# Optimization experiments

Measured on AMD Instinct MI355X. Metric: run time of the kernel, lower is better.

## Reference

```python
import jax, jax.numpy as jnp
import numpy as np


def setup_inputs() -> dict:
    key = jax.random.key(0)
    k1, k2, k3, k4 = jax.random.split(key, 4)
    B, M, S, Q = 128, 200, 20, 20
    H, V, D = 3, 50000, 128  # max_hops, num_vocab, embedding_dim
    story = jax.random.randint(k1, (B, M, S), 0, V)
    query = jax.random.randint(k2, (B, Q), 0, V)
    # (max_hops+1) embedding tables, init normal(0, 0.1) as in torch code
    E = jax.random.normal(k3, (H + 1, V, D), dtype=jnp.float32) * 0.1
    # (max_hops+1) temporal encodings [max_story_size, D], normal(0, 0.1)
    T = jax.random.normal(k4, (H + 1, M, D), dtype=jnp.float32) * 0.1
    return {"story": story, "query": query, "E": E, "T": T}


def reference(story, query, E, T):
    max_hops = E.shape[0] - 1
    # u1 = sum over query tokens of B-embedding (hop-0 table)
    u = jnp.sum(E[0][query], axis=1)  # [B, D]
    for hop in range(max_hops):
        # memory: A-embed story, sum over words, add temporal encoding
        m = jnp.sum(E[hop][story], axis=2) + T[hop]        # [B, M, D]
        # attention over memories (legacy F.softmax on 2D -> dim=1)
        uTm = jnp.einsum('bmd,bd->bm', m, u)               # [B, M]
        proba = jax.nn.softmax(uTm, axis=1)
        # output memory representation
        c = jnp.sum(E[hop + 1][story], axis=2) + T[hop + 1]  # [B, M, D]
        o = jnp.einsum('bm,bmd->bd', proba, c)             # [B, D]
        u = u + o
    ahat = u @ E[-1].T  # [B, V]
    return ahat, jax.nn.softmax(ahat, axis=1)
```

## Files before the change

kernel.cpp:

```cpp
#include <hip/hip_runtime.h>
#include <float.h>


constexpr int Bn = 128;
constexpr int Mn = 200;
constexpr int Sn = 20;
constexpr int Qn = 20;
constexpr int Hn = 3;
constexpr int Vn = 50000;
constexpr int Dn = 128;
constexpr int CH = 100;

constexpr size_t MSUM_ELEMS = (size_t)(Hn + 1) * Bn * Mn * Dn;

__global__ __launch_bounds__(256)
void msum_kernel(const int* __restrict__ story, const float* __restrict__ E,
                 const float* __restrict__ T, float* __restrict__ msum) {
    int slot = threadIdx.x >> 5;
    int l    = threadIdx.x & 31;
    int row  = blockIdx.x * 8 + slot;
    int t    = row / (Bn * Mn);
    int rem  = row - t * (Bn * Mn);
    int b    = rem / Mn;
    int m    = rem - b * Mn;

    const int* st = story + (b * Mn + m) * Sn;
    const float4* Tv = (const float4*)(T) + (size_t)(t * Mn + m) * 32;
    const float4* Et = (const float4*)(E) + (size_t)t * Vn * 32;

    float4 acc = Tv[l];
    #pragma unroll
    for (int s = 0; s < Sn; ++s) {
        float4 e = Et[(size_t)st[s] * 32 + l];
        acc.x += e.x; acc.y += e.y; acc.z += e.z; acc.w += e.w;
    }
    ((float4*)msum)[(size_t)row * 32 + l] = acc;
}

__global__ __launch_bounds__(1024)
void hops_kernel(const int* __restrict__ query, const float* __restrict__ E,
                 const float* __restrict__ msum, float* __restrict__ ufin) {
    __shared__ float u[Dn];
    __shared__ float sc[Mn];
    __shared__ float op[8 * Dn];
    __shared__ float red[16];
    __shared__ float bc[2];

    const int b    = blockIdx.x;
    const int tid  = threadIdx.x;
    const int wave = tid >> 6;
    const int lane = tid & 63;
    const int d    = tid & (Dn - 1);
    const int g    = tid >> 7;

    if (tid < Dn) {
        float acc = 0.f;
        const int* q = query + b * Qn;
        #pragma unroll
        for (int j = 0; j < Qn; ++j)
            acc += E[(size_t)q[j] * Dn + tid];
        u[tid] = acc;
    }
    __syncthreads();

    for (int hop = 0; hop < Hn; ++hop) {
        const float* mrow = msum + ((size_t)hop * Bn + b) * (size_t)(Mn * Dn);
        float ul = u[lane], uh = u[lane + 64];

        for (int mm = wave; mm < Mn / 2; mm += 16) {
            const float* r0 = mrow + (2 * mm) * Dn;
            const float* r1 = r0 + Dn;
            float p0 = r0[lane] * ul + r0[lane + 64] * uh;
            float p1 = r1[lane] * ul + r1[lane + 64] * uh;
            #pragma unroll
            for (int off = 32; off; off >>= 1) {
                p0 += __shfl_down(p0, off, 64);
                p1 += __shfl_down(p1, off, 64);
            }
            if (lane == 0) { sc[2 * mm] = p0; sc[2 * mm + 1] = p1; }
        }
        __syncthreads();

        float v = (tid < Mn) ? sc[tid] : -FLT_MAX;
        float mx = v;
        #pragma unroll
        for (int off = 32; off; off >>= 1) mx = fmaxf(mx, __shfl_down(mx, off, 64));
        if (lane == 0) red[wave] = mx;
        __syncthreads();
        if (tid == 0) {
            float m0 = red[0];
            #pragma unroll
            for (int i = 1; i < 16; ++i) m0 = fmaxf(m0, red[i]);
            bc[0] = m0;
        }
        __syncthreads();
        float rmax = bc[0];
        float e = (tid < Mn) ? expf(v - rmax) : 0.f;
        float sm = e;
        #pragma unroll
        for (int off = 32; off; off >>= 1) sm += __shfl_down(sm, off, 64);
        if (lane == 0) red[wave] = sm;
        __syncthreads();
        if (tid == 0) {
            float s = 0.f;
            #pragma unroll
            for (int i = 0; i < 16; ++i) s += red[i];
            bc[1] = s;
        }
        __syncthreads();
        float inv = 1.f / bc[1];
        if (tid < Mn) sc[tid] = e * inv;
        __syncthreads();

        const float* crow = msum + ((size_t)(hop + 1) * Bn + b) * (size_t)(Mn * Dn);
        float acc = 0.f;
        for (int m = g; m < Mn; m += 8)
            acc += sc[m] * crow[m * Dn + d];
        op[g * Dn + d] = acc;
        __syncthreads();
        if (tid < Dn) {
            float s = 0.f;
            #pragma unroll
            for (int i = 0; i < 8; ++i) s += op[i * Dn + tid];
            u[tid] += s;
        }
        __syncthreads();
    }
    if (tid < Dn) ufin[b * Dn + tid] = u[tid];
}

__global__ __launch_bounds__(1024)
void hops_fused_kernel(const int* __restrict__ story, const int* __restrict__ query,
                       const float* __restrict__ E, const float* __restrict__ T,
                       float* __restrict__ ufin) {
    __shared__ __align__(16) float tile[CH * Dn];
    __shared__ float u[Dn];
    __shared__ float sc[Mn];
    __shared__ float op[8 * Dn];
    __shared__ float red[16];
    __shared__ float bc[2];

    const int b    = blockIdx.x;
    const int tid  = threadIdx.x;
    const int wave = tid >> 6;
    const int lane = tid & 63;
    const int d    = tid & (Dn - 1);
    const int g    = tid >> 7;
    const int slot = tid >> 5;
    const int l    = tid & 31;
    const int* st  = story + b * (Mn * Sn);

    if (tid < Dn) {
        float acc = 0.f;
        const int* q = query + b * Qn;
        #pragma unroll
        for (int j = 0; j < Qn; ++j)
            acc += E[(size_t)q[j] * Dn + tid];
        u[tid] = acc;
    }

    auto build = [&](int t, int base) {
        const float4* Et = (const float4*)(E) + (size_t)t * Vn * 32;
        const float4* Tt = (const float4*)(T) + (size_t)t * Mn * 32;
        for (int m = base + slot; m < base + CH; m += 32) {
            const int* sm = st + m * Sn;
            float4 acc = Tt[(size_t)m * 32 + l];
            #pragma unroll
            for (int s = 0; s < Sn; ++s) {
                float4 e = Et[(size_t)sm[s] * 32 + l];
                acc.x += e.x; acc.y += e.y; acc.z += e.z; acc.w += e.w;
            }
            ((float4*)tile)[(m - base) * 32 + l] = acc;
        }
    };
    auto scores = [&](int base) {
        for (int m = base + wave; m < base + CH; m += 16) {
            float p = tile[(m - base) * Dn + lane]      * u[lane]
                    + tile[(m - base) * Dn + lane + 64] * u[lane + 64];
            #pragma unroll
            for (int off = 32; off; off >>= 1) p += __shfl_down(p, off, 64);
            if (lane == 0) sc[m] = p;
        }
    };

    for (int hop = 0; hop < Hn; ++hop) {
        if (hop == 0) {
            build(0, 0);  __syncthreads(); scores(0);  __syncthreads();
            build(0, CH); __syncthreads(); scores(CH); __syncthreads();
        } else {
            scores(CH); __syncthreads();
            build(hop, 0); __syncthreads(); scores(0); __syncthreads();
        }

        float v = (tid < Mn) ? sc[tid] : -FLT_MAX;
        float mx = v;
        #pragma unroll
        for (int off = 32; off; off >>= 1) mx = fmaxf(mx, __shfl_down(mx, off, 64));
        if (lane == 0) red[wave] = mx;
        __syncthreads();
        if (tid == 0) {
            float m0 = red[0];
            #pragma unroll
            for (int i = 1; i < 16; ++i) m0 = fmaxf(m0, red[i]);
            bc[0] = m0;
        }
        __syncthreads();
        float rmax = bc[0];
        float e = (tid < Mn) ? expf(v - rmax) : 0.f;
        float sm = e;
        #pragma unroll
        for (int off = 32; off; off >>= 1) sm += __shfl_down(sm, off, 64);
        if (lane == 0) red[wave] = sm;
        __syncthreads();
        if (tid == 0) {
            float s = 0.f;
            #pragma unroll
            for (int i = 0; i < 16; ++i) s += red[i];
            bc[1] = s;
        }
        __syncthreads();
        float inv = 1.f / bc[1];
        if (tid < Mn) sc[tid] = e * inv;

        float oacc = 0.f;
        build(hop + 1, 0);
        __syncthreads();
        for (int m = g; m < CH; m += 8)
            oacc += sc[m] * tile[m * Dn + d];
        __syncthreads();
        build(hop + 1, CH);
        __syncthreads();
        for (int m = CH + g; m < 2 * CH; m += 8)
            oacc += sc[m] * tile[(m - CH) * Dn + d];
        op[g * Dn + d] = oacc;
        __syncthreads();
        if (tid < Dn) {
            float s = 0.f;
            #pragma unroll
            for (int i = 0; i < 8; ++i) s += op[i * Dn + tid];
            u[tid] += s;
        }
        __syncthreads();
    }

    if (tid < Dn) ufin[b * Dn + tid] = u[tid];
}

constexpr int KC    = 32;
constexpr int LSTRA = 140;
constexpr int LSTRB = 72;
__device__ __forceinline__ int ldsCol(int c) { return c + 4 * (c >> 5); }

__global__ __launch_bounds__(256)
void ahat_gemm_kernel(const float* __restrict__ E, const float* __restrict__ ufin,
                      float* __restrict__ out) {
    __shared__ float uA[KC * LSTRA];
    __shared__ float eB[KC * LSTRB];
    const float* E3 = E + (size_t)Hn * Vn * Dn;

    const int tid   = threadIdx.x;
    const int tr    = tid & 15;
    const int tc    = tid >> 4;
    const int vbase = blockIdx.x * 64;

    const int f4 = tid & 7;
    const int rr = tid >> 3;

    float acc[8][4];
    #pragma unroll
    for (int i = 0; i < 8; ++i)
        #pragma unroll
        for (int j = 0; j < 4; ++j) acc[i][j] = 0.f;

    for (int kb = 0; kb < Dn; kb += KC) {
        #pragma unroll
        for (int i = 0; i < 4; ++i) {
            int r = rr + 32 * i;
            float4 uv = *(const float4*)(ufin + (size_t)r * Dn + kb + f4 * 4);
            int col = ldsCol(r);
            uA[(f4 * 4 + 0) * LSTRA + col] = uv.x;
            uA[(f4 * 4 + 1) * LSTRA + col] = uv.y;
            uA[(f4 * 4 + 2) * LSTRA + col] = uv.z;
            uA[(f4 * 4 + 3) * LSTRA + col] = uv.w;
        }
        #pragma unroll
        for (int i = 0; i < 2; ++i) {
            int r  = rr + 32 * i;
            int vg = vbase + r; if (vg > Vn - 1) vg = Vn - 1;
            float4 ev = *(const float4*)(E3 + (size_t)vg * Dn + kb + f4 * 4);
            int col = ldsCol(r);
            eB[(f4 * 4 + 0) * LSTRB + col] = ev.x;
            eB[(f4 * 4 + 1) * LSTRB + col] = ev.y;
            eB[(f4 * 4 + 2) * LSTRB + col] = ev.z;
            eB[(f4 * 4 + 3) * LSTRB + col] = ev.w;
        }
        __syncthreads();
        const int ca = ldsCol(tr * 8);
        const int cb = ldsCol(tc * 4);
        #pragma unroll 4
        for (int k = 0; k < KC; ++k) {
            float4 a0 = *(const float4*)&uA[k * LSTRA + ca];
            float4 a1 = *(const float4*)&uA[k * LSTRA + ca + 4];
            float4 b0 = *(const float4*)&eB[k * LSTRB + cb];
            float av[8] = {a0.x, a0.y, a0.z, a0.w, a1.x, a1.y, a1.z, a1.w};
            float bv[4] = {b0.x, b0.y, b0.z, b0.w};
            #pragma unroll
            for (int i = 0; i < 8; ++i)
                #pragma unroll
                for (int j = 0; j < 4; ++j)
                    acc[i][j] += av[i] * bv[j];
        }
        __syncthreads();
    }

    if (vbase + tc * 4 < Vn) {
        #pragma unroll
        for (int i = 0; i < 8; ++i) {
            int bb = tr * 8 + i;
            *(float4*)(out + (size_t)bb * Vn + vbase + tc * 4) =
                make_float4(acc[i][0], acc[i][1], acc[i][2], acc[i][3]);
        }
    }
}

__global__ __launch_bounds__(1024)
void softmax_kernel(const float* __restrict__ ahat, float* __restrict__ osm) {
    __shared__ float red[16];
    __shared__ float bc;

    int b    = blockIdx.x;
    int tid  = threadIdx.x;
    int wave = tid >> 6;
    int lane = tid & 63;

    const float4* row  = (const float4*)(ahat + (size_t)b * Vn);
    float4*       orow = (float4*)(osm + (size_t)b * Vn);
    constexpr int N4 = Vn / 4;

    float mx = -FLT_MAX;
    for (int v = tid; v < N4; v += 1024) {
        float4 x = row[v];
        mx = fmaxf(mx, fmaxf(fmaxf(x.x, x.y), fmaxf(x.z, x.w)));
    }
    #pragma unroll
    for (int off = 32; off; off >>= 1) mx = fmaxf(mx, __shfl_down(mx, off, 64));
    if (lane == 0) red[wave] = mx;
    __syncthreads();
    if (tid == 0) {
        float m = red[0];
        #pragma unroll
        for (int i = 1; i < 16; ++i) m = fmaxf(m, red[i]);
        bc = m;
    }
    __syncthreads();
    float rmax = bc;

    float sum = 0.f;
    for (int v = tid; v < N4; v += 1024) {
        float4 x = row[v];
        sum += expf(x.x - rmax) + expf(x.y - rmax) + expf(x.z - rmax) + expf(x.w - rmax);
    }
    #pragma unroll
    for (int off = 32; off; off >>= 1) sum += __shfl_down(sum, off, 64);
    if (lane == 0) red[wave] = sum;
    __syncthreads();
    if (tid == 0) {
        float s = 0.f;
        #pragma unroll
        for (int i = 0; i < 16; ++i) s += red[i];
        bc = s;
    }
    __syncthreads();
    float inv = 1.f / bc;

    for (int v = tid; v < N4; v += 1024) {
        float4 x = row[v];
        orow[v] = make_float4(expf(x.x - rmax) * inv, expf(x.y - rmax) * inv,
                              expf(x.z - rmax) * inv, expf(x.w - rmax) * inv);
    }
}

extern "C" void kernel_launch(void* const* d_in, const int* in_sizes, int n_in,
                              void* d_out, int out_size, void* d_ws, size_t ws_size,
                              hipStream_t stream) {
    const int*   story = (const int*)d_in[0];
    const int*   query = (const int*)d_in[1];
    const float* E     = (const float*)d_in[2];
    const float* T     = (const float*)d_in[3];

    float* out  = (float*)d_out;
    float* ufin = out + (size_t)Bn * Vn;

    if (ws_size >= MSUM_ELEMS * sizeof(float)) {
        float* msum = (float*)d_ws;
        msum_kernel<<<(Hn + 1) * Bn * Mn / 8, 256, 0, stream>>>(story, E, T, msum);
        hops_kernel<<<Bn, 1024, 0, stream>>>(query, E, msum, ufin);
    } else {
        hops_fused_kernel<<<Bn, 1024, 0, stream>>>(story, query, E, T, ufin);
    }
    ahat_gemm_kernel<<<(Vn + 63) / 64, 256, 0, stream>>>(E, ufin, out);
    softmax_kernel<<<Bn, 1024, 0, stream>>>(out, out + (size_t)Bn * Vn);
}
```

Measured before the change: 351.7 us.

## Split msum per table, widen GEMM tile, use online softmax

The msum gather is split into one launch per embedding table so each launch touches a single 25MB table, improving L2 locality, and it now uses vectorized nontemporal loads and stores for indices, T and the output. The ahat GEMM tile grows from 64 to 128 vocab columns with an 8x8 register micro-tile, giving more reuse per LDS load at the cost of more registers. The softmax fuses the max and sum passes into a single online pass with fast __expf, removing one full read of the logits. Risks are register pressure in the GEMM and slight accuracy changes from __expf.

```diff
diff --git a/kernel.cpp b/kernel.cpp
--- a/kernel.cpp
+++ b/kernel.cpp
@@ -13,28 +13,34 @@
 
 constexpr size_t MSUM_ELEMS = (size_t)(Hn + 1) * Bn * Mn * Dn;
 
+typedef float  f32x4 __attribute__((ext_vector_type(4)));
+typedef int    i32x4 __attribute__((ext_vector_type(4)));
+
 __global__ __launch_bounds__(256)
-void msum_kernel(const int* __restrict__ story, const float* __restrict__ E,
-                 const float* __restrict__ T, float* __restrict__ msum) {
+void msum_table_kernel(const int* __restrict__ story, const float4* __restrict__ Et,
+                       const float4* __restrict__ Tt, float4* __restrict__ msumT) {
     int slot = threadIdx.x >> 5;
     int l    = threadIdx.x & 31;
-    int row  = blockIdx.x * 8 + slot;
-    int t    = row / (Bn * Mn);
-    int rem  = row - t * (Bn * Mn);
-    int b    = rem / Mn;
-    int m    = rem - b * Mn;
-
-    const int* st = story + (b * Mn + m) * Sn;
-    const float4* Tv = (const float4*)(T) + (size_t)(t * Mn + m) * 32;
-    const float4* Et = (const float4*)(E) + (size_t)t * Vn * 32;
-
-    float4 acc = Tv[l];
+    int rbm  = blockIdx.x * 8 + slot;
+    int m    = rbm % Mn;
+
+    const i32x4* st4 = (const i32x4*)(story + (size_t)rbm * Sn);
+    i32x4 iv0 = __builtin_nontemporal_load(st4 + 0);
+    i32x4 iv1 = __builtin_nontemporal_load(st4 + 1);
+    i32x4 iv2 = __builtin_nontemporal_load(st4 + 2);
+    i32x4 iv3 = __builtin_nontemporal_load(st4 + 3);
+    i32x4 iv4 = __builtin_nontemporal_load(st4 + 4);
+    int idx[Sn] = {iv0.x, iv0.y, iv0.z, iv0.w, iv1.x, iv1.y, iv1.z, iv1.w,
+                   iv2.x, iv2.y, iv2.z, iv2.w, iv3.x, iv3.y, iv3.z, iv3.w,
+                   iv4.x, iv4.y, iv4.z, iv4.w};
+
+    f32x4 acc = __builtin_nontemporal_load((const f32x4*)Tt + (size_t)m * 32 + l);
     #pragma unroll
     for (int s = 0; s < Sn; ++s) {
-        float4 e = Et[(size_t)st[s] * 32 + l];
+        float4 e = Et[(size_t)idx[s] * 32 + l];
         acc.x += e.x; acc.y += e.y; acc.z += e.z; acc.w += e.w;
     }
-    ((float4*)msum)[(size_t)row * 32 + l] = acc;
+    __builtin_nontemporal_store(acc, (f32x4*)msumT + (size_t)rbm * 32 + l);
 }
 
 __global__ __launch_bounds__(1024)
@@ -246,87 +252,86 @@
     if (tid < Dn) ufin[b * Dn + tid] = u[tid];
 }
 
-constexpr int KC    = 32;
-constexpr int LSTRA = 140;
-constexpr int LSTRB = 72;
+constexpr int KC   = 32;
+constexpr int LSTR = 140;
 __device__ __forceinline__ int ldsCol(int c) { return c + 4 * (c >> 5); }
 
 __global__ __launch_bounds__(256)
 void ahat_gemm_kernel(const float* __restrict__ E, const float* __restrict__ ufin,
                       float* __restrict__ out) {
-    __shared__ float uA[KC * LSTRA];
-    __shared__ float eB[KC * LSTRB];
+    __shared__ float uA[KC * LSTR];
+    __shared__ float eB[KC * LSTR];
     const float* E3 = E + (size_t)Hn * Vn * Dn;
 
     const int tid   = threadIdx.x;
     const int tr    = tid & 15;
     const int tc    = tid >> 4;
-    const int vbase = blockIdx.x * 64;
+    const int vbase = blockIdx.x * 128;
 
     const int f4 = tid & 7;
     const int rr = tid >> 3;
 
-    float acc[8][4];
+    float acc[8][8];
     #pragma unroll
     for (int i = 0; i < 8; ++i)
         #pragma unroll
-        for (int j = 0; j < 4; ++j) acc[i][j] = 0.f;
+        for (int j = 0; j < 8; ++j) acc[i][j] = 0.f;
 
     for (int kb = 0; kb < Dn; kb += KC) {
         #pragma unroll
         for (int i = 0; i < 4; ++i) {
-            int r = rr + 32 * i;
+            int r   = rr + 32 * i;
+            int col = ldsCol(r);
             float4 uv = *(const float4*)(ufin + (size_t)r * Dn + kb + f4 * 4);
-            int col = ldsCol(r);
-            uA[(f4 * 4 + 0) * LSTRA + col] = uv.x;
-            uA[(f4 * 4 + 1) * LSTRA + col] = uv.y;
-            uA[(f4 * 4 + 2) * LSTRA + col] = uv.z;
-            uA[(f4 * 4 + 3) * LSTRA + col] = uv.w;
-        }
-        #pragma unroll
-        for (int i = 0; i < 2; ++i) {
-            int r  = rr + 32 * i;
+            uA[(f4 * 4 + 0) * LSTR + col] = uv.x;
+            uA[(f4 * 4 + 1) * LSTR + col] = uv.y;
+            uA[(f4 * 4 + 2) * LSTR + col] = uv.z;
+            uA[(f4 * 4 + 3) * LSTR + col] = uv.w;
             int vg = vbase + r; if (vg > Vn - 1) vg = Vn - 1;
             float4 ev = *(const float4*)(E3 + (size_t)vg * Dn + kb + f4 * 4);
-            int col = ldsCol(r);
-            eB[(f4 * 4 + 0) * LSTRB + col] = ev.x;
-            eB[(f4 * 4 + 1) * LSTRB + col] = ev.y;
-            eB[(f4 * 4 + 2) * LSTRB + col] = ev.z;
-            eB[(f4 * 4 + 3) * LSTRB + col] = ev.w;
+            eB[(f4 * 4 + 0) * LSTR + col] = ev.x;
+            eB[(f4 * 4 + 1) * LSTR + col] = ev.y;
+            eB[(f4 * 4 + 2) * LSTR + col] = ev.z;
+            eB[(f4 * 4 + 3) * LSTR + col] = ev.w;
         }
         __syncthreads();
         const int ca = ldsCol(tr * 8);
-        const int cb = ldsCol(tc * 4);
-        #pragma unroll 4
+        const int cb = ldsCol(tc * 8);
+        #pragma unroll 2
         for (int k = 0; k < KC; ++k) {
-            float4 a0 = *(const float4*)&uA[k * LSTRA + ca];
-            float4 a1 = *(const float4*)&uA[k * LSTRA + ca + 4];
-            float4 b0 = *(const float4*)&eB[k * LSTRB + cb];
+            float4 a0 = *(const float4*)&uA[k * LSTR + ca];
+            float4 a1 = *(const float4*)&uA[k * LSTR + ca + 4];
+            float4 b0 = *(const float4*)&eB[k * LSTR + cb];
+            float4 b1 = *(const float4*)&eB[k * LSTR + cb + 4];
             float av[8] = {a0.x, a0.y, a0.z, a0.w, a1.x, a1.y, a1.z, a1.w};
-            float bv[4] = {b0.x, b0.y, b0.z, b0.w};
+            float bv[8] = {b0.x, b0.y, b0.z, b0.w, b1.x, b1.y, b1.z, b1.w};
             #pragma unroll
             for (int i = 0; i < 8; ++i)
                 #pragma unroll
-                for (int j = 0; j < 4; ++j)
+                for (int j = 0; j < 8; ++j)
                     acc[i][j] += av[i] * bv[j];
         }
         __syncthreads();
     }
 
-    if (vbase + tc * 4 < Vn) {
+    const int v0 = vbase + tc * 8;
+    if (v0 < Vn) {
         #pragma unroll
         for (int i = 0; i < 8; ++i) {
             int bb = tr * 8 + i;
-            *(float4*)(out + (size_t)bb * Vn + vbase + tc * 4) =
+            *(float4*)(out + (size_t)bb * Vn + v0) =
                 make_float4(acc[i][0], acc[i][1], acc[i][2], acc[i][3]);
+            *(float4*)(out + (size_t)bb * Vn + v0 + 4) =
+                make_float4(acc[i][4], acc[i][5], acc[i][6], acc[i][7]);
         }
     }
 }
 
 __global__ __launch_bounds__(1024)
 void softmax_kernel(const float* __restrict__ ahat, float* __restrict__ osm) {
-    __shared__ float red[16];
-    __shared__ float bc;
+    __shared__ float redm[16];
+    __shared__ float reds[16];
+    __shared__ float bc2[2];
 
     int b    = blockIdx.x;
     int tid  = threadIdx.x;
@@ -337,46 +342,40 @@
     float4*       orow = (float4*)(osm + (size_t)b * Vn);
     constexpr int N4 = Vn / 4;
 
-    float mx = -FLT_MAX;
+    float m = -FLT_MAX, s = 0.f;
     for (int v = tid; v < N4; v += 1024) {
         float4 x = row[v];
-        mx = fmaxf(mx, fmaxf(fmaxf(x.x, x.y), fmaxf(x.z, x.w)));
+        float cm = fmaxf(fmaxf(x.x, x.y), fmaxf(x.z, x.w));
+        if (cm > m) { s *= __expf(m - cm); m = cm; }
+        s += __expf(x.x - m) + __expf(x.y - m) + __expf(x.z - m) + __expf(x.w - m);
     }
     #pragma unroll
-    for (int off = 32; off; off >>= 1) mx = fmaxf(mx, __shfl_down(mx, off, 64));
-    if (lane == 0) red[wave] = mx;
+    for (int off = 32; off; off >>= 1) {
+        float mo = __shfl_down(m, off, 64);
+        float so = __shfl_down(s, off, 64);
+        float nm = fmaxf(m, mo);
+        s = s * __expf(m - nm) + so * __expf(mo - nm);
+        m = nm;
+    }
+    if (lane == 0) { redm[wave] = m; reds[wave] = s; }
     __syncthreads();
     if (tid == 0) {
-        float m = red[0];
-        #pragma unroll
-        for (int i = 1; i < 16; ++i) m = fmaxf(m, red[i]);
-        bc = m;
+        float M = redm[0];
+        #pragma unroll
+        for (int i = 1; i < 16; ++i) M = fmaxf(M, redm[i]);
+        float S = 0.f;
+        #pragma unroll
+        for (int i = 0; i < 16; ++i) S += reds[i] * __expf(redm[i] - M);
+        bc2[0] = M; bc2[1] = 1.f / S;
     }
     __syncthreads();
-    float rmax = bc;
-
-    float sum = 0.f;
+    float rmax = bc2[0];
+    float inv  = bc2[1];
+
     for (int v = tid; v < N4; v += 1024) {
         float4 x = row[v];
-        sum += expf(x.x - rmax) + expf(x.y - rmax) + expf(x.z - rmax) + expf(x.w - rmax);
-    }
-    #pragma unroll
-    for (int off = 32; off; off >>= 1) sum += __shfl_down(sum, off, 64);
-    if (lane == 0) red[wave] = sum;
-    __syncthreads();
-    if (tid == 0) {
-        float s = 0.f;
-        #pragma unroll
-        for (int i = 0; i < 16; ++i) s += red[i];
-        bc = s;
-    }
-    __syncthreads();
-    float inv = 1.f / bc;
-
-    for (int v = tid; v < N4; v += 1024) {
-        float4 x = row[v];
-        orow[v] = make_float4(expf(x.x - rmax) * inv, expf(x.y - rmax) * inv,
-                              expf(x.z - rmax) * inv, expf(x.w - rmax) * inv);
+        orow[v] = make_float4(__expf(x.x - rmax) * inv, __expf(x.y - rmax) * inv,
+                              __expf(x.z - rmax) * inv, __expf(x.w - rmax) * inv);
     }
 }
 
@@ -393,11 +392,17 @@
 
     if (ws_size >= MSUM_ELEMS * sizeof(float)) {
         float* msum = (float*)d_ws;
-        msum_kernel<<<(Hn + 1) * Bn * Mn / 8, 256, 0, stream>>>(story, E, T, msum);
+        for (int t = 0; t < Hn + 1; ++t) {
+            msum_table_kernel<<<Bn * Mn / 8, 256, 0, stream>>>(
+                story,
+                (const float4*)(E + (size_t)t * Vn * Dn),
+                (const float4*)(T + (size_t)t * Mn * Dn),
+                (float4*)(msum + (size_t)t * Bn * Mn * Dn));
+        }
         hops_kernel<<<Bn, 1024, 0, stream>>>(query, E, msum, ufin);
     } else {
         hops_fused_kernel<<<Bn, 1024, 0, stream>>>(story, query, E, T, ufin);
     }
-    ahat_gemm_kernel<<<(Vn + 63) / 64, 256, 0, stream>>>(E, ufin, out);
+    ahat_gemm_kernel<<<(Vn + 127) / 128, 256, 0, stream>>>(E, ufin, out);
     softmax_kernel<<<Bn, 1024, 0, stream>>>(out, out + (size_t)Bn * Vn);
 }
```

After: 382.9 us. 1.09x slower.
